# Kernel optimization log

Hardware: AMD Instinct MI355X
Metric: run time of the kernel (lower is better)

## Reference

```python
import jax, jax.numpy as jnp
import numpy as np

GRID = 64
N_NODES = GRID * GRID
LN_EPS = 1e-5


def _grid_edge_index(n=GRID):
    ids = np.arange(n * n, dtype=np.int32).reshape(n, n)
    r0, r1 = ids[:, :-1].ravel(), ids[:, 1:].ravel()   # horizontal neighbors
    d0, d1 = ids[:-1, :].ravel(), ids[1:, :].ravel()   # vertical neighbors
    src = np.concatenate([r0, r1, d0, d1])
    dst = np.concatenate([r1, r0, d1, d0])
    return np.stack([src, dst])  # [2, 16128] directed edges


def setup_inputs() -> dict:
    key = jax.random.key(0)
    ks = jax.random.split(key, 6)
    B, C, H, L = 128, 12, 64, 3
    s_in = 1.0 / np.sqrt(C)
    s_h = 1.0 / np.sqrt(H)
    return {
        "x": jax.random.normal(ks[0], (B, C, GRID, GRID), jnp.float32),
        "edge_index": jnp.asarray(_grid_edge_index()),
        "w_in": jax.random.normal(ks[1], (C, H), jnp.float32) * s_in,
        "b_in": jnp.zeros((H,), jnp.float32),
        "w_self": jax.random.normal(ks[2], (L, H, H), jnp.float32) * s_h,
        "w_neigh": jax.random.normal(ks[3], (L, H, H), jnp.float32) * s_h,
        "conv_b": jnp.zeros((L, H), jnp.float32),
        "ln_g": jnp.ones((L, H), jnp.float32),
        "ln_b": jnp.zeros((L, H), jnp.float32),
        "w_head": jax.random.normal(ks[4], (H, 1), jnp.float32) * s_h,
        "b_head": jnp.zeros((1,), jnp.float32),
    }


def reference(x, edge_index, w_in, b_in, w_self, w_neigh, conv_b, ln_g, ln_b, w_head, b_head):
    B = x.shape[0]
    BN = B * N_NODES
    # grid_to_nodes: [B, C, 64, 64] -> [B, N, C]
    nodes = jnp.transpose(x, (0, 2, 3, 1)).reshape(B, N_NODES, -1)
    h = (nodes @ w_in + b_in).reshape(BN, -1)
    # batched_edge_index: replicate with per-graph node offsets
    offs = (jnp.arange(B, dtype=edge_index.dtype) * N_NODES)
    ei = (edge_index[:, None, :] + offs[None, :, None]).reshape(2, -1)
    src, dst = ei[0], ei[1]
    deg = jax.ops.segment_sum(jnp.ones_like(src, dtype=h.dtype), dst, num_segments=BN)
    inv_deg = (1.0 / jnp.maximum(deg, 1.0))[:, None]
    n_layers = w_self.shape[0]
    for l in range(n_layers):
        # SAGE-mean conv: gather src feats, scatter-sum to dst, mean-normalize
        agg = jax.ops.segment_sum(h[src], dst, num_segments=BN) * inv_deg
        hn = h @ w_self[l] + agg @ w_neigh[l] + conv_b[l]
        mu = hn.mean(-1, keepdims=True)
        var = ((hn - mu) ** 2).mean(-1, keepdims=True)
        hn = (hn - mu) * jax.lax.rsqrt(var + LN_EPS) * ln_g[l] + ln_b[l]
        h = h + jax.nn.relu(hn)  # dropout is identity in eval mode
    logit = (h @ w_head + b_head).reshape(B, GRID, GRID)
    return logit
```

## Files before the change

kernel.cpp:

```cpp
#include <hip/hip_runtime.h>

#define GRID_D 64
#define NN (GRID_D * GRID_D)
#define H 64
#define C_IN 12
#define B_SZ 128
#define LN_EPS 1e-5f

typedef _Float16 f16x8 __attribute__((ext_vector_type(8)));
typedef _Float16 f16x4 __attribute__((ext_vector_type(4)));
typedef float    f32x4 __attribute__((ext_vector_type(4)));

#define AS1 __attribute__((address_space(1)))
#define AS3 __attribute__((address_space(3)))

__global__ __launch_bounds__(256) void k_inproj(
    const float* __restrict__ x, const float* __restrict__ w_in,
    const float* __restrict__ b_in, _Float16* __restrict__ h,
    const float* __restrict__ ws_, const float* __restrict__ wn_,
    _Float16* __restrict__ wt)
{
    int bid = blockIdx.x;
    int b = bid >> 6, r = bid & 63;
    int tid = threadIdx.x;

    int pi = bid * 256 + tid;
    if (pi < 3 * 2 * 4096) {
        int l = pi >> 13, g = (pi >> 12) & 1, j = (pi >> 6) & 63, k = pi & 63;
        const float* W = (g ? wn_ : ws_) + l * 4096;
        wt[pi] = (_Float16)W[k * 64 + j];
    }

    __shared__ float xs[C_IN][GRID_D];
    __shared__ float ws[C_IN][H];
    const float* xb = x + (size_t)b * C_IN * NN + (size_t)r * GRID_D;
    for (int idx = tid; idx < C_IN * GRID_D; idx += 256) {
        int c = idx >> 6, n = idx & 63;
        xs[c][n] = xb[(size_t)c * NN + n];
        ws[c][n] = w_in[idx];
    }
    __syncthreads();
    int n = tid >> 2;
    int j0 = (tid & 3) * 16;
    float acc[16];
    #pragma unroll
    for (int t = 0; t < 16; ++t) acc[t] = b_in[j0 + t];
    #pragma unroll
    for (int c = 0; c < C_IN; ++c) {
        float xv = xs[c][n];
        #pragma unroll
        for (int t = 0; t < 16; ++t) acc[t] += xv * ws[c][j0 + t];
    }
    _Float16* hp = h + (size_t)(b * NN + r * GRID_D + n) * H + j0;
    f16x8 o0, o1;
    #pragma unroll
    for (int t = 0; t < 8; ++t) { o0[t] = (_Float16)acc[t]; o1[t] = (_Float16)acc[8 + t]; }
    *(f16x8*)hp = o0;
    *(f16x8*)(hp + 8) = o1;
}

__device__ __forceinline__ void stage_row(
    const _Float16* hb, int grow, _Float16* slot, int wv, int ln)
{
    const _Float16* src = hb
        + (((size_t)(grow * GRID_D + wv * 8 + (ln >> 3))) << 6)
        + (((ln & 7) ^ (ln >> 3)) << 3);
    _Float16* dst = slot + wv * 512;
    __builtin_amdgcn_global_load_lds((const AS1 void*)src, (AS3 void*)dst, 16, 0, 0);
}

__global__ __launch_bounds__(768, 3) void k_fused(
    const _Float16* __restrict__ h0, float* __restrict__ logits,
    const _Float16* __restrict__ wtb,
    const float* __restrict__ cb, const float* __restrict__ lg,
    const float* __restrict__ lb,
    const float* __restrict__ w_head, const float* __restrict__ b_head)
{
    __shared__ _Float16 ring[3][4][4096];
    __shared__ float    pl[640];

    int tid = threadIdx.x, ln = tid & 63, wv = tid >> 6;
    int bid = blockIdx.x;
    int img = bid >> 1, chunk = bid & 1;
    int r0 = chunk << 5;
    const _Float16* hb = h0 + ((size_t)img << 18);

    int grp = wv >> 2;
    int ct  = wv & 3;
    int lrow = ln & 15, kgrp = ln >> 4;
    int col = ct * 16 + lrow;
    int cs = col & 7;
    int kq = kgrp * 4;
    bool cl = (col > 0), cr = (col < 63);

    const _Float16* wg = wtb + grp * 8192;
    f16x8 wsf[2][4], wnf[2][4];
    #pragma unroll
    for (int ks = 0; ks < 2; ++ks) {
        int k0 = ks * 32 + kq * 2;
        #pragma unroll
        for (int ft = 0; ft < 4; ++ft) {
            int j = ft * 16 + lrow;
            wsf[ks][ft] = *(const f16x8*)(wg + (j << 6) + k0);
            wnf[ks][ft] = *(const f16x8*)(wg + ((64 + j) << 6) + k0);
        }
    }
    #pragma unroll
    for (int ks = 0; ks < 2; ++ks)
        #pragma unroll
        for (int ft = 0; ft < 4; ++ft)
            asm volatile("" : "+v"(wsf[ks][ft]), "+v"(wnf[ks][ft]));

    if (tid < 576) {
        int l = tid / 192, r = tid % 192;
        pl[tid] = (r < 64) ? cb[l * 64 + r]
                : (r < 128) ? lg[l * 64 + r - 64] : lb[l * 64 + r - 128];
    } else if (tid < 640) {
        pl[tid] = w_head[tid - 576];
    }

    const float* myp = pl + grp * 192;
    float bh = b_head[0];

    int lo0 = (r0 - 3 < 0) ? 0 : r0 - 3, hi0 = (r0 + 34 > 63) ? 63 : r0 + 34;
    int loC, hiC;
    if (grp == 0)      { loC = (r0 - 2 < 0) ? 0 : r0 - 2; hiC = (r0 + 33 > 63) ? 63 : r0 + 33; }
    else if (grp == 1) { loC = (r0 - 1 < 0) ? 0 : r0 - 1; hiC = (r0 + 32 > 63) ? 63 : r0 + 32; }
    else               { loC = r0;                         hiC = r0 + 31; }

    _Float16* rin  = &ring[grp][0][0];
    _Float16* rout = (grp < 2) ? &ring[grp + 1][0][0] : nullptr;

    #pragma unroll 1
    for (int s = 0; s <= 40; ++s) {
        int p0 = r0 - 3 + s;
        if (wv < 8 && p0 >= lo0 && p0 <= hi0)
            stage_row(hb, p0, &ring[0][p0 & 3][0], wv, ln);

        int pr = p0 - 2 * grp - 2;
        if (pr >= loC && pr <= hiC) {
            const _Float16* rc = rin + ((pr & 3) << 12);
            const _Float16* ru = rin + (((pr - 1) & 3) << 12);
            const _Float16* rd = rin + (((pr + 1) & 3) << 12);
            _Float16 hinv = (_Float16)(1.0f / (float)((pr > 0) + (pr < 63) + cl + cr));

            f32x4 acc[4];
            #pragma unroll
            for (int ft = 0; ft < 4; ++ft) acc[ft] = (f32x4){0.f, 0.f, 0.f, 0.f};

            __builtin_amdgcn_s_setprio(1);
            #pragma unroll
            for (int ks = 0; ks < 2; ++ks) {
                int sl = ((ks * 4 + kgrp) ^ cs) << 3;
                f16x8 a = *(const f16x8*)(rc + (col << 6) + sl);
                #pragma unroll
                for (int ft = 0; ft < 4; ++ft)
                    acc[ft] = __builtin_amdgcn_mfma_f32_16x16x32_f16(wsf[ks][ft], a, acc[ft], 0, 0, 0);
            }

            #pragma unroll
            for (int ks = 0; ks < 2; ++ks) {
                int c8 = ks * 4 + kgrp;
                int sl = (c8 ^ cs) << 3;
                f16x8 z = {};
                f16x8 u = (pr > 0)  ? *(const f16x8*)(ru + (col << 6) + sl) : z;
                f16x8 d = (pr < 63) ? *(const f16x8*)(rd + (col << 6) + sl) : z;
                int cm = col - cl;
                f16x8 lv = *(const f16x8*)(rc + (cm << 6) + ((c8 ^ (cm & 7)) << 3));
                if (!cl) lv = z;
                int cp = col + cr;
                f16x8 rv = *(const f16x8*)(rc + (cp << 6) + ((c8 ^ (cp & 7)) << 3));
                if (!cr) rv = z;
                f16x8 sm = (lv + rv) + (u + d);
                f16x8 g;
                #pragma unroll
                for (int e = 0; e < 8; ++e) g[e] = sm[e] * hinv;
                #pragma unroll
                for (int ft = 0; ft < 4; ++ft)
                    acc[ft] = __builtin_amdgcn_mfma_f32_16x16x32_f16(wnf[ks][ft], g, acc[ft], 0, 0, 0);
            }
            __builtin_amdgcn_s_setprio(0);

            float s1 = 0.f, s2 = 0.f;
            #pragma unroll
            for (int ft = 0; ft < 4; ++ft) {
                f32x4 q = *(const f32x4*)&myp[ft * 16 + kq];
                acc[ft] += q;
                #pragma unroll
                for (int t = 0; t < 4; ++t) { float xv = acc[ft][t]; s1 += xv; s2 += xv * xv; }
            }
            s1 += __shfl_xor(s1, 16); s1 += __shfl_xor(s1, 32);
            s2 += __shfl_xor(s2, 16); s2 += __shfl_xor(s2, 32);
            float mu   = s1 * (1.0f / H);
            float var  = s2 * (1.0f / H) - mu * mu;
            float rstd = rsqrtf(var + LN_EPS);

            const _Float16* res = rc + (col << 6);
            if (grp < 2) {
                _Float16* outp = rout + ((pr & 3) << 12) + (col << 6);
                #pragma unroll
                for (int ft = 0; ft < 4; ++ft) {
                    f32x4 lgq = *(const f32x4*)&myp[64 + ft * 16 + kq];
                    f32x4 lbq = *(const f32x4*)&myp[128 + ft * 16 + kq];
                    int slot = (ft * 2 + (kgrp >> 1)) ^ cs;
                    f16x4 rq = *(const f16x4*)(res + (slot << 3) + (kgrp & 1) * 4);
                    f16x4 oq;
                    #pragma unroll
                    for (int t = 0; t < 4; ++t) {
                        float o = (float)rq[t]
                                + fmaxf((acc[ft][t] - mu) * rstd * lgq[t] + lbq[t], 0.f);
                        oq[t] = (_Float16)o;
                    }
                    *(f16x4*)(outp + (slot << 3) + (kgrp & 1) * 4) = oq;
                }
            } else {
                float part = 0.f;
                #pragma unroll
                for (int ft = 0; ft < 4; ++ft) {
                    f32x4 lgq = *(const f32x4*)&myp[64 + ft * 16 + kq];
                    f32x4 lbq = *(const f32x4*)&myp[128 + ft * 16 + kq];
                    f32x4 whq = *(const f32x4*)&pl[576 + ft * 16 + kq];
                    int slot = (ft * 2 + (kgrp >> 1)) ^ cs;
                    f16x4 rq = *(const f16x4*)(res + (slot << 3) + (kgrp & 1) * 4);
                    #pragma unroll
                    for (int t = 0; t < 4; ++t) {
                        float o = (float)rq[t]
                                + fmaxf((acc[ft][t] - mu) * rstd * lgq[t] + lbq[t], 0.f);
                        part += o * whq[t];
                    }
                }
                part += __shfl_xor(part, 16);
                part += __shfl_xor(part, 32);
                if (kgrp == 0)
                    logits[(size_t)img * NN + pr * GRID_D + col] = part + bh;
            }
        }
        __syncthreads();
    }
}

extern "C" void kernel_launch(void* const* d_in, const int* in_sizes, int n_in,
                              void* d_out, int out_size, void* d_ws, size_t ws_size,
                              hipStream_t stream) {
    const float* x      = (const float*)d_in[0];
    const float* w_in   = (const float*)d_in[2];
    const float* b_in   = (const float*)d_in[3];
    const float* w_self = (const float*)d_in[4];
    const float* w_neigh= (const float*)d_in[5];
    const float* conv_b = (const float*)d_in[6];
    const float* ln_g   = (const float*)d_in[7];
    const float* ln_b   = (const float*)d_in[8];
    const float* w_head = (const float*)d_in[9];
    const float* b_head = (const float*)d_in[10];
    float* out = (float*)d_out;

    char* base = (char*)d_ws;
    const size_t HBYTES = (size_t)B_SZ * NN * H * sizeof(_Float16);
    _Float16* h_a = (_Float16*)base;
    _Float16* wtb = (_Float16*)(base + HBYTES);

    k_inproj<<<B_SZ * GRID_D, 256, 0, stream>>>(
        x, w_in, b_in, h_a, w_self, w_neigh, wtb);
    k_fused<<<B_SZ * 2, 768, 0, stream>>>(
        h_a, out, wtb, conv_b, ln_g, ln_b, w_head, b_head);
}
```

Before: 107.5 us.

## Process two rows per barrier step with deeper LDS ring buffers

The fused 3-layer wavefront loop now stages two input rows and computes two rows per layer group per iteration, roughly halving the number of __syncthreads barriers. The ring buffers grow from 4 slots to 7/6/6 slots with modular slot indices tracked incrementally. The cost is more LDS use, which may lower occupancy below the declared 3 blocks per CU, and a longer pipeline skew per group.

```diff
diff --git a/kernel.cpp b/kernel.cpp
--- a/kernel.cpp
+++ b/kernel.cpp
@@ -13,6 +13,8 @@
 
 #define AS1 __attribute__((address_space(1)))
 #define AS3 __attribute__((address_space(3)))
+
+__device__ __forceinline__ int pmod(int a, int m) { int r = a % m; return r < 0 ? r + m : r; }
 
 __global__ __launch_bounds__(256) void k_inproj(
     const float* __restrict__ x, const float* __restrict__ w_in,
@@ -76,7 +78,9 @@
     const float* __restrict__ lb,
     const float* __restrict__ w_head, const float* __restrict__ b_head)
 {
-    __shared__ _Float16 ring[3][4][4096];
+    __shared__ _Float16 ring0[7 * 4096];
+    __shared__ _Float16 ring1[6 * 4096];
+    __shared__ _Float16 ring2[6 * 4096];
     __shared__ float    pl[640];
 
     int tid = threadIdx.x, ln = tid & 63, wv = tid >> 6;
@@ -128,113 +132,142 @@
     else if (grp == 1) { loC = (r0 - 1 < 0) ? 0 : r0 - 1; hiC = (r0 + 32 > 63) ? 63 : r0 + 32; }
     else               { loC = r0;                         hiC = r0 + 31; }
 
-    _Float16* rin  = &ring[grp][0][0];
-    _Float16* rout = (grp < 2) ? &ring[grp + 1][0][0] : nullptr;
+    const _Float16* rin = (grp == 0) ? ring0 : (grp == 1) ? ring1 : ring2;
+    _Float16* rout      = (grp == 0) ? ring1 : ring2;
+    int Nin = (grp == 0) ? 7 : 6;
+
+    int qb = r0 - 9 - 3 * grp;
+    int rs0 = pmod(qb - 1, Nin), rs1 = pmod(qb, Nin);
+    int rs2 = pmod(qb + 1, Nin), rs3 = pmod(qb + 2, Nin);
+    int ws0 = pmod(qb, 6), ws1 = pmod(qb + 1, 6);
+    int st0 = pmod(r0 - 5, 7), st1 = pmod(r0 - 4, 7);
 
     #pragma unroll 1
-    for (int s = 0; s <= 40; ++s) {
-        int p0 = r0 - 3 + s;
-        if (wv < 8 && p0 >= lo0 && p0 <= hi0)
-            stage_row(hb, p0, &ring[0][p0 & 3][0], wv, ln);
-
-        int pr = p0 - 2 * grp - 2;
-        if (pr >= loC && pr <= hiC) {
-            const _Float16* rc = rin + ((pr & 3) << 12);
-            const _Float16* ru = rin + (((pr - 1) & 3) << 12);
-            const _Float16* rd = rin + (((pr + 1) & 3) << 12);
-            _Float16 hinv = (_Float16)(1.0f / (float)((pr > 0) + (pr < 63) + cl + cr));
-
-            f32x4 acc[4];
-            #pragma unroll
-            for (int ft = 0; ft < 4; ++ft) acc[ft] = (f32x4){0.f, 0.f, 0.f, 0.f};
-
-            __builtin_amdgcn_s_setprio(1);
-            #pragma unroll
-            for (int ks = 0; ks < 2; ++ks) {
-                int sl = ((ks * 4 + kgrp) ^ cs) << 3;
-                f16x8 a = *(const f16x8*)(rc + (col << 6) + sl);
-                #pragma unroll
-                for (int ft = 0; ft < 4; ++ft)
-                    acc[ft] = __builtin_amdgcn_mfma_f32_16x16x32_f16(wsf[ks][ft], a, acc[ft], 0, 0, 0);
-            }
-
-            #pragma unroll
-            for (int ks = 0; ks < 2; ++ks) {
-                int c8 = ks * 4 + kgrp;
-                int sl = (c8 ^ cs) << 3;
-                f16x8 z = {};
-                f16x8 u = (pr > 0)  ? *(const f16x8*)(ru + (col << 6) + sl) : z;
-                f16x8 d = (pr < 63) ? *(const f16x8*)(rd + (col << 6) + sl) : z;
-                int cm = col - cl;
-                f16x8 lv = *(const f16x8*)(rc + (cm << 6) + ((c8 ^ (cm & 7)) << 3));
-                if (!cl) lv = z;
-                int cp = col + cr;
-                f16x8 rv = *(const f16x8*)(rc + (cp << 6) + ((c8 ^ (cp & 7)) << 3));
-                if (!cr) rv = z;
-                f16x8 sm = (lv + rv) + (u + d);
-                f16x8 g;
-                #pragma unroll
-                for (int e = 0; e < 8; ++e) g[e] = sm[e] * hinv;
-                #pragma unroll
-                for (int ft = 0; ft < 4; ++ft)
-                    acc[ft] = __builtin_amdgcn_mfma_f32_16x16x32_f16(wnf[ks][ft], g, acc[ft], 0, 0, 0);
-            }
-            __builtin_amdgcn_s_setprio(0);
-
-            float s1 = 0.f, s2 = 0.f;
-            #pragma unroll
-            for (int ft = 0; ft < 4; ++ft) {
-                f32x4 q = *(const f32x4*)&myp[ft * 16 + kq];
-                acc[ft] += q;
-                #pragma unroll
-                for (int t = 0; t < 4; ++t) { float xv = acc[ft][t]; s1 += xv; s2 += xv * xv; }
-            }
-            s1 += __shfl_xor(s1, 16); s1 += __shfl_xor(s1, 32);
-            s2 += __shfl_xor(s2, 16); s2 += __shfl_xor(s2, 32);
-            float mu   = s1 * (1.0f / H);
-            float var  = s2 * (1.0f / H) - mu * mu;
-            float rstd = rsqrtf(var + LN_EPS);
-
-            const _Float16* res = rc + (col << 6);
-            if (grp < 2) {
-                _Float16* outp = rout + ((pr & 3) << 12) + (col << 6);
+    for (int s = 0; s <= 23; ++s) {
+        int P = r0 - 5 + 2 * s;
+        if (wv < 8) {
+            if (P >= lo0 && P <= hi0)
+                stage_row(hb, P, ring0 + (st0 << 12), wv, ln);
+            if (P + 1 >= lo0 && P + 1 <= hi0)
+                stage_row(hb, P + 1, ring0 + (st1 << 12), wv, ln);
+        }
+
+        #pragma unroll
+        for (int rr = 0; rr < 2; ++rr) {
+            int q = qb + rr;
+            int sA = rr ? rs1 : rs0;
+            int sB = rr ? rs2 : rs1;
+            int sC = rr ? rs3 : rs2;
+            int sW = rr ? ws1 : ws0;
+            if (q >= loC && q <= hiC) {
+                const _Float16* rc = rin + (sB << 12);
+                const _Float16* ru = rin + (sA << 12);
+                const _Float16* rd = rin + (sC << 12);
+                _Float16 hinv = (_Float16)(1.0f / (float)((q > 0) + (q < 63) + cl + cr));
+
+                f32x4 acc[4];
+                #pragma unroll
+                for (int ft = 0; ft < 4; ++ft) acc[ft] = (f32x4){0.f, 0.f, 0.f, 0.f};
+
+                __builtin_amdgcn_s_setprio(1);
+                #pragma unroll
+                for (int ks = 0; ks < 2; ++ks) {
+                    int sl = ((ks * 4 + kgrp) ^ cs) << 3;
+                    f16x8 a = *(const f16x8*)(rc + (col << 6) + sl);
+                    #pragma unroll
+                    for (int ft = 0; ft < 4; ++ft)
+                        acc[ft] = __builtin_amdgcn_mfma_f32_16x16x32_f16(wsf[ks][ft], a, acc[ft], 0, 0, 0);
+                }
+
+                #pragma unroll
+                for (int ks = 0; ks < 2; ++ks) {
+                    int c8 = ks * 4 + kgrp;
+                    int sl = (c8 ^ cs) << 3;
+                    f16x8 z = {};
+                    f16x8 u = (q > 0)  ? *(const f16x8*)(ru + (col << 6) + sl) : z;
+                    f16x8 d = (q < 63) ? *(const f16x8*)(rd + (col << 6) + sl) : z;
+                    int cm = col - cl;
+                    f16x8 lv = *(const f16x8*)(rc + (cm << 6) + ((c8 ^ (cm & 7)) << 3));
+                    if (!cl) lv = z;
+                    int cp = col + cr;
+                    f16x8 rv = *(const f16x8*)(rc + (cp << 6) + ((c8 ^ (cp & 7)) << 3));
+                    if (!cr) rv = z;
+                    f16x8 sm = (lv + rv) + (u + d);
+                    f16x8 g;
+                    #pragma unroll
+                    for (int e = 0; e < 8; ++e) g[e] = sm[e] * hinv;
+                    #pragma unroll
+                    for (int ft = 0; ft < 4; ++ft)
+                        acc[ft] = __builtin_amdgcn_mfma_f32_16x16x32_f16(wnf[ks][ft], g, acc[ft], 0, 0, 0);
+                }
+                __builtin_amdgcn_s_setprio(0);
+
+                float s1 = 0.f, s2 = 0.f;
                 #pragma unroll
                 for (int ft = 0; ft < 4; ++ft) {
-                    f32x4 lgq = *(const f32x4*)&myp[64 + ft * 16 + kq];
-                    f32x4 lbq = *(const f32x4*)&myp[128 + ft * 16 + kq];
-                    int slot = (ft * 2 + (kgrp >> 1)) ^ cs;
-                    f16x4 rq = *(const f16x4*)(res + (slot << 3) + (kgrp & 1) * 4);
-                    f16x4 oq;
-                    #pragma unroll
-                    for (int t = 0; t < 4; ++t) {
-                        float o = (float)rq[t]
-                                + fmaxf((acc[ft][t] - mu) * rstd * lgq[t] + lbq[t], 0.f);
-                        oq[t] = (_Float16)o;
+                    f32x4 qv = *(const f32x4*)&myp[ft * 16 + kq];
+                    acc[ft] += qv;
+                    #pragma unroll
+                    for (int t = 0; t < 4; ++t) { float xv = acc[ft][t]; s1 += xv; s2 += xv * xv; }
+                }
+                s1 += __shfl_xor(s1, 16); s1 += __shfl_xor(s1, 32);
+                s2 += __shfl_xor(s2, 16); s2 += __shfl_xor(s2, 32);
+                float mu   = s1 * (1.0f / H);
+                float var  = s2 * (1.0f / H) - mu * mu;
+                float rstd = rsqrtf(var + LN_EPS);
+
+                const _Float16* res = rc + (col << 6);
+                if (grp < 2) {
+                    _Float16* outp = rout + (sW << 12) + (col << 6);
+                    #pragma unroll
+                    for (int ft = 0; ft < 4; ++ft) {
+                        f32x4 lgq = *(const f32x4*)&myp[64 + ft * 16 + kq];
+                        f32x4 lbq = *(const f32x4*)&myp[128 + ft * 16 + kq];
+                        int slot = (ft * 2 + (kgrp >> 1)) ^ cs;
+                        f16x4 rq = *(const f16x4*)(res + (slot << 3) + (kgrp & 1) * 4);
+                        f16x4 oq;
+                        #pragma unroll
+                        for (int t = 0; t < 4; ++t) {
+                            float o = (float)rq[t]
+                                    + fmaxf((acc[ft][t] - mu) * rstd * lgq[t] + lbq[t], 0.f);
+                            oq[t] = (_Float16)o;
+                        }
+                        *(f16x4*)(outp + (slot << 3) + (kgrp & 1) * 4) = oq;
                     }
-                    *(f16x4*)(outp + (slot << 3) + (kgrp & 1) * 4) = oq;
-                }
-            } else {
-                float part = 0.f;
-                #pragma unroll
-                for (int ft = 0; ft < 4; ++ft) {
-                    f32x4 lgq = *(const f32x4*)&myp[64 + ft * 16 + kq];
-                    f32x4 lbq = *(const f32x4*)&myp[128 + ft * 16 + kq];
-                    f32x4 whq = *(const f32x4*)&pl[576 + ft * 16 + kq];
-                    int slot = (ft * 2 + (kgrp >> 1)) ^ cs;
-                    f16x4 rq = *(const f16x4*)(res + (slot << 3) + (kgrp & 1) * 4);
-                    #pragma unroll
-                    for (int t = 0; t < 4; ++t) {
-                        float o = (float)rq[t]
-                                + fmaxf((acc[ft][t] - mu) * rstd * lgq[t] + lbq[t], 0.f);
-                        part += o * whq[t];
+                } else {
+                    float part = 0.f;
+                    #pragma unroll
+                    for (int ft = 0; ft < 4; ++ft) {
+                        f32x4 lgq = *(const f32x4*)&myp[64 + ft * 16 + kq];
+                        f32x4 lbq = *(const f32x4*)&myp[128 + ft * 16 + kq];
+                        f32x4 whq = *(const f32x4*)&pl[576 + ft * 16 + kq];
+                        int slot = (ft * 2 + (kgrp >> 1)) ^ cs;
+                        f16x4 rq = *(const f16x4*)(res + (slot << 3) + (kgrp & 1) * 4);
+                        #pragma unroll
+                        for (int t = 0; t < 4; ++t) {
+                            float o = (float)rq[t]
+                                    + fmaxf((acc[ft][t] - mu) * rstd * lgq[t] + lbq[t], 0.f);
+                            part += o * whq[t];
+                        }
                     }
-                }
-                part += __shfl_xor(part, 16);
-                part += __shfl_xor(part, 32);
-                if (kgrp == 0)
-                    logits[(size_t)img * NN + pr * GRID_D + col] = part + bh;
+                    part += __shfl_xor(part, 16);
+                    part += __shfl_xor(part, 32);
+                    if (kgrp == 0)
+                        logits[(size_t)img * NN + q * GRID_D + col] = part + bh;
+                }
             }
         }
+
+        rs0 += 2; if (rs0 >= Nin) rs0 -= Nin;
+        rs1 += 2; if (rs1 >= Nin) rs1 -= Nin;
+        rs2 += 2; if (rs2 >= Nin) rs2 -= Nin;
+        rs3 += 2; if (rs3 >= Nin) rs3 -= Nin;
+        ws0 += 2; if (ws0 >= 6) ws0 -= 6;
+        ws1 += 2; if (ws1 >= 6) ws1 -= 6;
+        st0 += 2; if (st0 >= 7) st0 -= 7;
+        st1 += 2; if (st1 >= 7) st1 -= 7;
+        qb += 2;
+
         __syncthreads();
     }
 }
```

Result: no change. 107.6 us (+0.0%).

## Prefetch input rows one step ahead with 5-slot ring and partial vmcnt wait

Applied to the files above, without the earlier changes.

Stage 0's input ring grows from 4 to 5 row slots, and the global-to-LDS load for row S runs one iteration ahead of consumption, with the first row prefetched at s==0. The end-of-iteration __syncthreads becomes an explicit s_waitcnt vmcnt(1) plus s_barrier, so the newest prefetch can stay in flight across the barrier. This hides global load latency behind the MFMA/LayerNorm work of the current row. It adds LDS usage, which may reduce occupancy, and it depends on vmcnt ordering being correct so the layer-0 reads see completed data.

```diff
diff --git a/kernel.cpp b/kernel.cpp
--- a/kernel.cpp
+++ b/kernel.cpp
@@ -13,6 +13,8 @@
 
 #define AS1 __attribute__((address_space(1)))
 #define AS3 __attribute__((address_space(3)))
+
+__device__ __forceinline__ int pmod(int a, int m) { int r = a % m; return r < 0 ? r + m : r; }
 
 __global__ __launch_bounds__(256) void k_inproj(
     const float* __restrict__ x, const float* __restrict__ w_in,
@@ -76,7 +78,9 @@
     const float* __restrict__ lb,
     const float* __restrict__ w_head, const float* __restrict__ b_head)
 {
-    __shared__ _Float16 ring[3][4][4096];
+    __shared__ _Float16 ring0[5 * 4096];
+    __shared__ _Float16 ring1[4 * 4096];
+    __shared__ _Float16 ring2[4 * 4096];
     __shared__ float    pl[640];
 
     int tid = threadIdx.x, ln = tid & 63, wv = tid >> 6;
@@ -128,20 +132,36 @@
     else if (grp == 1) { loC = (r0 - 1 < 0) ? 0 : r0 - 1; hiC = (r0 + 32 > 63) ? 63 : r0 + 32; }
     else               { loC = r0;                         hiC = r0 + 31; }
 
-    _Float16* rin  = &ring[grp][0][0];
-    _Float16* rout = (grp < 2) ? &ring[grp + 1][0][0] : nullptr;
+    const _Float16* rin = (grp == 0) ? ring0 : (grp == 1) ? ring1 : ring2;
+    _Float16* rout      = (grp == 0) ? ring1 : ring2;
+
+    int a0 = pmod(r0 - 6, 5), a1 = pmod(r0 - 5, 5), a2 = pmod(r0 - 4, 5);
+    int stS = pmod(r0 - 2, 5);
 
     #pragma unroll 1
     for (int s = 0; s <= 40; ++s) {
+        int S = r0 - 2 + s;
+        bool do_stage = (S >= lo0 && S <= hi0);
+        if (wv < 8) {
+            if (s == 0 && r0 - 3 >= 0)
+                stage_row(hb, r0 - 3, ring0 + (pmod(r0 - 3, 5) << 12), wv, ln);
+            if (do_stage)
+                stage_row(hb, S, ring0 + (stS << 12), wv, ln);
+        }
+
         int p0 = r0 - 3 + s;
-        if (wv < 8 && p0 >= lo0 && p0 <= hi0)
-            stage_row(hb, p0, &ring[0][p0 & 3][0], wv, ln);
-
         int pr = p0 - 2 * grp - 2;
         if (pr >= loC && pr <= hiC) {
-            const _Float16* rc = rin + ((pr & 3) << 12);
-            const _Float16* ru = rin + (((pr - 1) & 3) << 12);
-            const _Float16* rd = rin + (((pr + 1) & 3) << 12);
+            const _Float16 *rc, *ru, *rd;
+            if (grp == 0) {
+                rc = ring0 + (a1 << 12);
+                ru = ring0 + (a0 << 12);
+                rd = ring0 + (a2 << 12);
+            } else {
+                rc = rin + ((pr & 3) << 12);
+                ru = rin + (((pr - 1) & 3) << 12);
+                rd = rin + (((pr + 1) & 3) << 12);
+            }
             _Float16 hinv = (_Float16)(1.0f / (float)((pr > 0) + (pr < 63) + cl + cr));
 
             f32x4 acc[4];
@@ -235,7 +255,16 @@
                     logits[(size_t)img * NN + pr * GRID_D + col] = part + bh;
             }
         }
-        __syncthreads();
+
+        a0 += 1; if (a0 >= 5) a0 -= 5;
+        a1 += 1; if (a1 >= 5) a1 -= 5;
+        a2 += 1; if (a2 >= 5) a2 -= 5;
+        stS += 1; if (stS >= 5) stS -= 5;
+
+        if (do_stage)
+            asm volatile("s_waitcnt vmcnt(1) lgkmcnt(0)\n\ts_barrier" ::: "memory");
+        else
+            asm volatile("s_waitcnt vmcnt(0) lgkmcnt(0)\n\ts_barrier" ::: "memory");
     }
 }
 
```

Measured after the change: 111.7 us. +3.9%, slower.
